# Kernel tuning notes

Hardware: AMD Instinct MI355X
Metric: run time of the kernel (lower is better)

The kernel has to match this reference:

```python
import jax, jax.numpy as jnp
import numpy as np

EPS = 1e-5

def mean_normalization(feat):
    # per (batch, channel) statistics over spatial dims, unbiased variance (torch default)
    mean = jnp.mean(feat, axis=(2, 3), keepdims=True)
    var = jnp.var(feat, axis=(2, 3), keepdims=True, ddof=1)
    return (feat - mean) / jnp.sqrt(var + EPS)

def setup_inputs() -> dict:
    key = jax.random.key(0)
    ks = jax.random.split(key, 8)
    B, C, H, W = 4, 512, 64, 64
    fan = np.sqrt(6.0 / (C + C))  # xavier_uniform gain=1 for 1x1 conv
    return {
        "content_feat": jax.random.normal(ks[0], (B, C, H, W), jnp.float32),
        "style_feat": jax.random.normal(ks[1], (B, C, H, W), jnp.float32),
        "Wq": jax.random.uniform(ks[2], (C, C), jnp.float32, -fan, fan),
        "bq": jax.random.uniform(ks[3], (C,), jnp.float32, 0.0, 1.0),
        "Wk": jax.random.uniform(ks[4], (C, C), jnp.float32, -fan, fan),
        "bk": jax.random.uniform(ks[5], (C,), jnp.float32, 0.0, 1.0),
        "Wv": jax.random.uniform(ks[6], (C, C), jnp.float32, -fan, fan),
        "bv": jax.random.uniform(ks[7], (C,), jnp.float32, 0.0, 1.0),
    }

def reference(content_feat, style_feat, Wq, bq, Wk, bk, Wv, bv):
    B, C, H, W = content_feat.shape
    N = H * W
    # 1x1 convs == channel-mixing GEMMs
    Q = jnp.einsum('oc,bchw->bohw', Wq, mean_normalization(content_feat)) + bq[None, :, None, None]
    K = jnp.einsum('oc,bchw->bohw', Wk, mean_normalization(style_feat)) + bk[None, :, None, None]
    V = jnp.einsum('oc,bchw->bohw', Wv, style_feat) + bv[None, :, None, None]
    Q = Q.reshape(B, C, N)              # [B, C, Nq]
    K = K.reshape(B, C, N)              # [B, C, Nk]
    V = V.reshape(B, C, N)              # [B, C, Nk]
    # scores[b, n, m] = Q^T K  (no 1/sqrt(d) scaling, per original)
    scores = jnp.einsum('bcn,bcm->bnm', Q, K)
    A = jax.nn.softmax(scores, axis=-1)             # [B, Nq, Nk]
    Out = jnp.einsum('bcm,bnm->bcn', V, A)          # V @ A^T
    return Out.reshape(B, C, H, W)
```

## Files before the change

kernel.cpp:

```cpp
#include <hip/hip_runtime.h>

typedef _Float16 f16;
typedef _Float16 f16x4 __attribute__((ext_vector_type(4)));
typedef _Float16 f16x8 __attribute__((ext_vector_type(8)));
typedef float f32x4 __attribute__((ext_vector_type(4)));

#define MFMA16(a, b, c) __builtin_amdgcn_mfma_f32_16x16x32_f16(a, b, c, 0, 0, 0)

__global__ __launch_bounds__(256) void stats_kernel(
    const float* __restrict__ content, const float* __restrict__ style,
    float* __restrict__ mu, float* __restrict__ rs)
{
    int bid = blockIdx.x;
    int tensor = bid >> 11;
    int row = bid & 2047;
    const float* src = (tensor ? style : content) + (size_t)row * 4096;
    int t = threadIdx.x;
    float s = 0.f, ss = 0.f;
    for (int i = t; i < 1024; i += 256) {
        float4 v = reinterpret_cast<const float4*>(src)[i];
        s  += v.x + v.y + v.z + v.w;
        ss += v.x * v.x + v.y * v.y + v.z * v.z + v.w * v.w;
    }
    for (int off = 32; off > 0; off >>= 1) {
        s  += __shfl_down(s, off);
        ss += __shfl_down(ss, off);
    }
    __shared__ float sb[4], ssb[4];
    int wv = t >> 6;
    if ((t & 63) == 0) { sb[wv] = s; ssb[wv] = ss; }
    __syncthreads();
    if (t == 0) {
        float S  = sb[0] + sb[1] + sb[2] + sb[3];
        float SS = ssb[0] + ssb[1] + ssb[2] + ssb[3];
        float m  = S * (1.f / 4096.f);
        float var = (SS - 4096.f * m * m) * (1.f / 4095.f);
        mu[bid] = m;
        rs[bid] = rsqrtf(var + 1e-5f);
    }
}

__global__ __launch_bounds__(256) void qkv_kernel(
    const float* __restrict__ content, const float* __restrict__ style,
    const float* __restrict__ Wq, const float* __restrict__ bq,
    const float* __restrict__ Wk, const float* __restrict__ bk,
    const float* __restrict__ Wv, const float* __restrict__ bv,
    const float* __restrict__ mu, const float* __restrict__ rs,
    f16* __restrict__ Qt, f16* __restrict__ Kt, f16* __restrict__ Vc)
{
    int z = blockIdx.z;
    int b = z / 3, p = z % 3;
    int n0 = blockIdx.x * 128;
    int o0 = blockIdx.y * 128;
    const float* X    = (p == 0 ? content : style) + (size_t)b * 512 * 4096;
    const float* W    = (p == 0 ? Wq : (p == 1 ? Wk : Wv));
    const float* bias = (p == 0 ? bq : (p == 1 ? bk : bv));
    const float* muT = mu + (p == 0 ? 0 : 2048) + b * 512;
    const float* rsT = rs + (p == 0 ? 0 : 2048) + b * 512;
    bool norm = (p < 2);

    __shared__ __align__(16) f16 Xt[128][40];
    __shared__ __align__(16) f16 Wl[128][40];

    int t = threadIdx.x;
    int lane = t & 63, w = t >> 6;
    int wn = (w & 1) * 64, wo = (w >> 1) * 64;
    int lg = lane >> 4, li = lane & 15;

    f32x4 acc[4][4];
#pragma unroll
    for (int i = 0; i < 4; ++i)
#pragma unroll
        for (int j = 0; j < 4; ++j)
#pragma unroll
            for (int e = 0; e < 4; ++e) acc[i][j][e] = 0.f;

    for (int kk = 0; kk < 16; ++kk) {
        int c0 = kk * 32;
        __syncthreads();
#pragma unroll
        for (int r = 0; r < 4; ++r) {
            int linear = r * 256 + t;
            int c  = linear >> 5;
            int nq = linear & 31;
            float4 v = reinterpret_cast<const float4*>(X + (size_t)(c0 + c) * 4096 + n0)[nq];
            float m = 0.f, sc = 1.f;
            if (norm) { m = muT[c0 + c]; sc = rsT[c0 + c]; }
            int n = nq * 4;
            Xt[n + 0][c] = (f16)((v.x - m) * sc);
            Xt[n + 1][c] = (f16)((v.y - m) * sc);
            Xt[n + 2][c] = (f16)((v.z - m) * sc);
            Xt[n + 3][c] = (f16)((v.w - m) * sc);
        }
#pragma unroll
        for (int r = 0; r < 4; ++r) {
            int linear = r * 256 + t;
            int o  = linear >> 3;
            int cq = linear & 7;
            float4 v = reinterpret_cast<const float4*>(W + (size_t)(o0 + o) * 512 + c0)[cq];
            int c = cq * 4;
            Wl[o][c + 0] = (f16)v.x;
            Wl[o][c + 1] = (f16)v.y;
            Wl[o][c + 2] = (f16)v.z;
            Wl[o][c + 3] = (f16)v.w;
        }
        __syncthreads();

        f16x8 xf[4], wf[4];
#pragma unroll
        for (int f = 0; f < 4; ++f) {
            xf[f] = *reinterpret_cast<const f16x8*>(&Xt[wn + f * 16 + li][lg * 8]);
            wf[f] = *reinterpret_cast<const f16x8*>(&Wl[wo + f * 16 + li][lg * 8]);
        }
        if (p < 2) {
#pragma unroll
            for (int i = 0; i < 4; ++i)
#pragma unroll
                for (int j = 0; j < 4; ++j)
                    acc[i][j] = MFMA16(wf[i], xf[j], acc[i][j]);
        } else {
#pragma unroll
            for (int i = 0; i < 4; ++i)
#pragma unroll
                for (int j = 0; j < 4; ++j)
                    acc[i][j] = MFMA16(xf[i], wf[j], acc[i][j]);
        }
    }

    if (p < 2) {
        f16* dst = (p == 0 ? Qt : Kt) + (size_t)b * 4096 * 512;
#pragma unroll
        for (int i = 0; i < 4; ++i) {
            int ob = o0 + wo + i * 16 + lg * 4;
            float4 bb = *reinterpret_cast<const float4*>(bias + ob);
#pragma unroll
            for (int j = 0; j < 4; ++j) {
                int n = n0 + wn + j * 16 + li;
                f16x4 pk;
                pk[0] = (f16)(acc[i][j][0] + bb.x);
                pk[1] = (f16)(acc[i][j][1] + bb.y);
                pk[2] = (f16)(acc[i][j][2] + bb.z);
                pk[3] = (f16)(acc[i][j][3] + bb.w);
                *reinterpret_cast<f16x4*>(dst + (size_t)n * 512 + ob) = pk;
            }
        }
    } else {
#pragma unroll
        for (int j = 0; j < 4; ++j) {
            int o = o0 + wo + j * 16 + li;
            float bb = bias[o];
            f16* dst = Vc + ((size_t)b * 512 + o) * 4096;
#pragma unroll
            for (int i = 0; i < 4; ++i) {
                int n = n0 + wn + i * 16 + lg * 4;
                f16x4 pk;
#pragma unroll
                for (int e = 0; e < 4; ++e) pk[e] = (f16)(acc[i][j][e] + bb);
                *reinterpret_cast<f16x4*>(dst + n) = pk;
            }
        }
    }
}

__global__ __launch_bounds__(768, 3) void attn_kernel(
    const f16* __restrict__ Qt, const f16* __restrict__ Kt,
    const f16* __restrict__ Vc, float* __restrict__ out)
{
    int bid = blockIdx.x;
    int orig = (bid & 7) * 32 + (bid >> 3);
    int b = orig >> 6;
    int n0 = (orig & 63) * 64;

    int t = threadIdx.x;
    int lane = t & 63, w = t >> 6;
    int lg = lane >> 4, li = lane & 15;

    __shared__ __align__(16) f16 Km[2][64][528];
    __shared__ __align__(16) f16 Pl[2][64][68];
    __shared__ __align__(16) float Rrow[2][64];
    __shared__ __align__(16) float Lrow[64];
    __shared__ int Rflag[2][4];

    const f16* Qb = Qt + (size_t)b * 4096 * 512;
    const f16* Kb = Kt + (size_t)b * 4096 * 512;
    const f16* Vb = Vc + (size_t)b * 512 * 4096;

    if (w < 4) {
        int j = w;
        f16x8 qf[16];
#pragma unroll
        for (int kk = 0; kk < 16; ++kk)
            qf[kk] = *reinterpret_cast<const f16x8*>(
                Qb + (size_t)(n0 + j * 16 + li) * 512 + kk * 32 + lg * 8);

#define STAGEK(TILE)                                                           \
        {                                                                      \
            int _db = (TILE) & 1;                                              \
            _Pragma("unroll")                                                  \
            for (int r = 0; r < 16; ++r) {                                     \
                const f16* _gs = Kb + ((size_t)(TILE) * 64 + j * 16 + r) * 512 \
                                 + lane * 8;                                   \
                __builtin_amdgcn_global_load_lds(                              \
                    (const __attribute__((address_space(1))) void*)_gs,        \
                    (__attribute__((address_space(3))) void*)&Km[_db][j * 16 + r][0], \
                    16, 0, 0);                                                 \
            }                                                                  \
        }

        STAGEK(0);
        float Mreg = -3.4e38f, Lreg = 0.f;
        __syncthreads();

        for (int it = 0; it <= 64; ++it) {
            if (it <= 63) {
                int cur = it & 1;
                if (it < 63) STAGEK(it + 1);

                f32x4 s[4];
#pragma unroll
                for (int mg = 0; mg < 4; ++mg)
#pragma unroll
                    for (int e = 0; e < 4; ++e) s[mg][e] = 0.f;
                __builtin_amdgcn_s_setprio(1);
#pragma unroll
                for (int kk = 0; kk < 16; ++kk) {
#pragma unroll
                    for (int mg = 0; mg < 4; ++mg) {
                        f16x8 kf = *reinterpret_cast<const f16x8*>(
                            &Km[cur][mg * 16 + li][kk * 32 + lg * 8]);
                        s[mg] = MFMA16(kf, qf[kk], s[mg]);
                    }
                }
                __builtin_amdgcn_s_setprio(0);

                float mx = s[0][0];
#pragma unroll
                for (int mg = 0; mg < 4; ++mg)
#pragma unroll
                    for (int e = 0; e < 4; ++e) mx = fmaxf(mx, s[mg][e]);
                mx = fmaxf(mx, __shfl_xor(mx, 16));
                mx = fmaxf(mx, __shfl_xor(mx, 32));
                bool needR = (mx - Mreg) > 4.0f;
                float Mnew = needR ? mx : Mreg;
                float r = needR ? __expf(Mreg - Mnew) : 1.f;
                float p[4][4];
                float sum = 0.f;
#pragma unroll
                for (int mg = 0; mg < 4; ++mg)
#pragma unroll
                    for (int e = 0; e < 4; ++e) {
                        p[mg][e] = __expf(s[mg][e] - Mnew);
                        sum += p[mg][e];
                    }
                sum += __shfl_xor(sum, 16);
                sum += __shfl_xor(sum, 32);
                Lreg = Lreg * r + sum;
                Mreg = Mnew;

#pragma unroll
                for (int mg = 0; mg < 4; ++mg) {
                    f16x4 pk;
#pragma unroll
                    for (int e = 0; e < 4; ++e) pk[e] = (f16)p[mg][e];
                    *reinterpret_cast<f16x4*>(&Pl[cur][j * 16 + li][mg * 16 + lg * 4]) = pk;
                }
                if (lg == 0) Rrow[cur][j * 16 + li] = r;
                int any = __any(needR);
                if (lane == 0) Rflag[cur][j] = any;
                if (it == 63 && lg == 0) Lrow[j * 16 + li] = Lreg;
            }
            __syncthreads();
        }
#undef STAGEK
    } else {
        int pw = w - 4;
        int c0 = pw * 64;
        f32x4 acc[4][4];
#pragma unroll
        for (int fn = 0; fn < 4; ++fn)
#pragma unroll
            for (int fc = 0; fc < 4; ++fc)
#pragma unroll
                for (int e = 0; e < 4; ++e) acc[fn][fc][e] = 0.f;
        f16x8 vfr[4][2];

        __syncthreads();

        for (int it = 0; it <= 64; ++it) {
            if (it >= 1) {
                int pp = (it - 1) & 1;
                if (Rflag[pp][0] | Rflag[pp][1] | Rflag[pp][2] | Rflag[pp][3]) {
#pragma unroll
                    for (int fn = 0; fn < 4; ++fn) {
                        f32x4 rv = *reinterpret_cast<const f32x4*>(&Rrow[pp][fn * 16 + lg * 4]);
#pragma unroll
                        for (int fc = 0; fc < 4; ++fc)
#pragma unroll
                            for (int e = 0; e < 4; ++e) acc[fn][fc][e] *= rv[e];
                    }
                }
                __builtin_amdgcn_s_setprio(1);
#pragma unroll
                for (int fn = 0; fn < 4; ++fn) {
                    f16x8 af0 = *reinterpret_cast<const f16x8*>(&Pl[pp][fn * 16 + li][lg * 8]);
                    f16x8 af1 = *reinterpret_cast<const f16x8*>(&Pl[pp][fn * 16 + li][32 + lg * 8]);
#pragma unroll
                    for (int fc = 0; fc < 4; ++fc) {
                        acc[fn][fc] = MFMA16(af0, vfr[fc][0], acc[fn][fc]);
                        acc[fn][fc] = MFMA16(af1, vfr[fc][1], acc[fn][fc]);
                    }
                }
                __builtin_amdgcn_s_setprio(0);
            }
            if (it <= 63) {
                const f16* vs = Vb + (size_t)(c0 + li) * 4096 + it * 64 + lg * 8;
#pragma unroll
                for (int fc = 0; fc < 4; ++fc) {
                    vfr[fc][0] = *reinterpret_cast<const f16x8*>(vs + (size_t)fc * 16 * 4096);
                    vfr[fc][1] = *reinterpret_cast<const f16x8*>(vs + (size_t)fc * 16 * 4096 + 32);
                }
            }
            __syncthreads();
        }

        float* ob = out + (size_t)b * 512 * 4096;
#pragma unroll
        for (int fn = 0; fn < 4; ++fn) {
            f32x4 lv = *reinterpret_cast<const f32x4*>(&Lrow[fn * 16 + lg * 4]);
            f32x4 linv;
#pragma unroll
            for (int e = 0; e < 4; ++e) linv[e] = 1.f / lv[e];
#pragma unroll
            for (int fc = 0; fc < 4; ++fc) {
                int c = c0 + fc * 16 + li;
                f32x4 o4;
#pragma unroll
                for (int e = 0; e < 4; ++e) o4[e] = acc[fn][fc][e] * linv[e];
                *reinterpret_cast<f32x4*>(ob + (size_t)c * 4096 + n0 + fn * 16 + lg * 4) = o4;
            }
        }
    }
}

extern "C" void kernel_launch(void* const* d_in, const int* in_sizes, int n_in,
                              void* d_out, int out_size, void* d_ws, size_t ws_size,
                              hipStream_t stream)
{
    const float* content = (const float*)d_in[0];
    const float* style   = (const float*)d_in[1];
    const float* Wq = (const float*)d_in[2];
    const float* bq = (const float*)d_in[3];
    const float* Wk = (const float*)d_in[4];
    const float* bk = (const float*)d_in[5];
    const float* Wv = (const float*)d_in[6];
    const float* bv = (const float*)d_in[7];
    float* out = (float*)d_out;

    const size_t TEN = (size_t)4 * 4096 * 512;
    f16* Qt = (f16*)d_ws;
    f16* Kt = Qt + TEN;
    f16* Vc = Kt + TEN;
    float* mu = (float*)(Vc + TEN);
    float* rs = mu + 4096;

    hipLaunchKernelGGL(stats_kernel, dim3(4096), dim3(256), 0, stream,
                       content, style, mu, rs);
    hipLaunchKernelGGL(qkv_kernel, dim3(32, 4, 12), dim3(256), 0, stream,
                       content, style, Wq, bq, Wk, bk, Wv, bv, mu, rs, Qt, Kt, Vc);
    hipLaunchKernelGGL(attn_kernel, dim3(256), dim3(768), 0, stream,
                       Qt, Kt, Vc, out);
}
```

Measured before the change: 302.0 us.

## Pre-convert weights to fp16 and restructure QKV GEMM to stage full-K activation tile

Adds a kernel that converts Wq/Wk/Wv to fp16 once per call. The QKV projection now has each block handle 64 spatial positions across all 512 output channels. The block loads the whole normalized 64x512 activation tile into shared memory once, and each wave streams fp16 weight fragments straight from global memory. This removes the per-K-step shared-memory staging, the repeated fp32 weight conversion and the per-iteration barriers. The costs are an extra launch, weight reads served from global/L2 instead of shared memory, and a larger shared allocation that may limit occupancy.

```diff
diff --git a/kernel.cpp b/kernel.cpp
--- a/kernel.cpp
+++ b/kernel.cpp
@@ -40,33 +40,69 @@
     }
 }
 
-__global__ __launch_bounds__(256) void qkv_kernel(
+__global__ __launch_bounds__(256) void wcvt_kernel(
+    const float* __restrict__ Wq, const float* __restrict__ Wk,
+    const float* __restrict__ Wv, f16* __restrict__ Wh)
+{
+    int p = blockIdx.y;
+    const float* W = (p == 0 ? Wq : (p == 1 ? Wk : Wv));
+    f16* dst = Wh + (size_t)p * 262144;
+    int base = blockIdx.x * 256 + threadIdx.x;
+#pragma unroll
+    for (int i = 0; i < 8; ++i) {
+        int e4 = i * 8192 + base;
+        float4 v = reinterpret_cast<const float4*>(W)[e4];
+        f16x4 pk;
+        pk[0] = (f16)v.x; pk[1] = (f16)v.y; pk[2] = (f16)v.z; pk[3] = (f16)v.w;
+        reinterpret_cast<f16x4*>(dst)[e4] = pk;
+    }
+}
+
+__global__ __launch_bounds__(512, 3) void qkv_kernel(
     const float* __restrict__ content, const float* __restrict__ style,
-    const float* __restrict__ Wq, const float* __restrict__ bq,
-    const float* __restrict__ Wk, const float* __restrict__ bk,
-    const float* __restrict__ Wv, const float* __restrict__ bv,
+    const f16* __restrict__ Wh,
+    const float* __restrict__ bq, const float* __restrict__ bk,
+    const float* __restrict__ bv,
     const float* __restrict__ mu, const float* __restrict__ rs,
     f16* __restrict__ Qt, f16* __restrict__ Kt, f16* __restrict__ Vc)
 {
-    int z = blockIdx.z;
-    int b = z / 3, p = z % 3;
-    int n0 = blockIdx.x * 128;
-    int o0 = blockIdx.y * 128;
+    int nb = blockIdx.x;
+    int y  = blockIdx.y;
+    int b = y / 3, p = y % 3;
+    int n0 = nb * 64;
     const float* X    = (p == 0 ? content : style) + (size_t)b * 512 * 4096;
-    const float* W    = (p == 0 ? Wq : (p == 1 ? Wk : Wv));
+    const f16*   Wp   = Wh + (size_t)p * 262144;
     const float* bias = (p == 0 ? bq : (p == 1 ? bk : bv));
-    const float* muT = mu + (p == 0 ? 0 : 2048) + b * 512;
-    const float* rsT = rs + (p == 0 ? 0 : 2048) + b * 512;
+    const float* muT  = mu + (p == 0 ? 0 : 2048) + b * 512;
+    const float* rsT  = rs + (p == 0 ? 0 : 2048) + b * 512;
     bool norm = (p < 2);
 
-    __shared__ __align__(16) f16 Xt[128][40];
-    __shared__ __align__(16) f16 Wl[128][40];
+    __shared__ __align__(16) f16 Xt[64][520];
 
     int t = threadIdx.x;
     int lane = t & 63, w = t >> 6;
-    int wn = (w & 1) * 64, wo = (w >> 1) * 64;
     int lg = lane >> 4, li = lane & 15;
 
+#pragma unroll
+    for (int i = 0; i < 16; ++i) {
+        int c0 = i * 32 + w * 4;
+        float x0 = X[(size_t)(c0 + 0) * 4096 + n0 + lane];
+        float x1 = X[(size_t)(c0 + 1) * 4096 + n0 + lane];
+        float x2 = X[(size_t)(c0 + 2) * 4096 + n0 + lane];
+        float x3 = X[(size_t)(c0 + 3) * 4096 + n0 + lane];
+        f16x4 pk;
+        if (norm) {
+            pk[0] = (f16)((x0 - muT[c0 + 0]) * rsT[c0 + 0]);
+            pk[1] = (f16)((x1 - muT[c0 + 1]) * rsT[c0 + 1]);
+            pk[2] = (f16)((x2 - muT[c0 + 2]) * rsT[c0 + 2]);
+            pk[3] = (f16)((x3 - muT[c0 + 3]) * rsT[c0 + 3]);
+        } else {
+            pk[0] = (f16)x0; pk[1] = (f16)x1; pk[2] = (f16)x2; pk[3] = (f16)x3;
+        }
+        *reinterpret_cast<f16x4*>(&Xt[lane][c0]) = pk;
+    }
+    __syncthreads();
+
     f32x4 acc[4][4];
 #pragma unroll
     for (int i = 0; i < 4; ++i)
@@ -75,87 +111,59 @@
 #pragma unroll
             for (int e = 0; e < 4; ++e) acc[i][j][e] = 0.f;
 
+    const f16* wbase = Wp + (size_t)(w * 64 + li) * 512 + lg * 8;
     for (int kk = 0; kk < 16; ++kk) {
-        int c0 = kk * 32;
-        __syncthreads();
-#pragma unroll
-        for (int r = 0; r < 4; ++r) {
-            int linear = r * 256 + t;
-            int c  = linear >> 5;
-            int nq = linear & 31;
-            float4 v = reinterpret_cast<const float4*>(X + (size_t)(c0 + c) * 4096 + n0)[nq];
-            float m = 0.f, sc = 1.f;
-            if (norm) { m = muT[c0 + c]; sc = rsT[c0 + c]; }
-            int n = nq * 4;
-            Xt[n + 0][c] = (f16)((v.x - m) * sc);
-            Xt[n + 1][c] = (f16)((v.y - m) * sc);
-            Xt[n + 2][c] = (f16)((v.z - m) * sc);
-            Xt[n + 3][c] = (f16)((v.w - m) * sc);
-        }
-#pragma unroll
-        for (int r = 0; r < 4; ++r) {
-            int linear = r * 256 + t;
-            int o  = linear >> 3;
-            int cq = linear & 7;
-            float4 v = reinterpret_cast<const float4*>(W + (size_t)(o0 + o) * 512 + c0)[cq];
-            int c = cq * 4;
-            Wl[o][c + 0] = (f16)v.x;
-            Wl[o][c + 1] = (f16)v.y;
-            Wl[o][c + 2] = (f16)v.z;
-            Wl[o][c + 3] = (f16)v.w;
-        }
-        __syncthreads();
-
         f16x8 xf[4], wf[4];
 #pragma unroll
-        for (int f = 0; f < 4; ++f) {
-            xf[f] = *reinterpret_cast<const f16x8*>(&Xt[wn + f * 16 + li][lg * 8]);
-            wf[f] = *reinterpret_cast<const f16x8*>(&Wl[wo + f * 16 + li][lg * 8]);
-        }
+        for (int jn = 0; jn < 4; ++jn)
+            xf[jn] = *reinterpret_cast<const f16x8*>(&Xt[jn * 16 + li][kk * 32 + lg * 8]);
+#pragma unroll
+        for (int io = 0; io < 4; ++io)
+            wf[io] = *reinterpret_cast<const f16x8*>(wbase + (size_t)io * 16 * 512 + kk * 32);
         if (p < 2) {
 #pragma unroll
-            for (int i = 0; i < 4; ++i)
-#pragma unroll
-                for (int j = 0; j < 4; ++j)
-                    acc[i][j] = MFMA16(wf[i], xf[j], acc[i][j]);
+            for (int io = 0; io < 4; ++io)
+#pragma unroll
+                for (int jn = 0; jn < 4; ++jn)
+                    acc[io][jn] = MFMA16(wf[io], xf[jn], acc[io][jn]);
         } else {
 #pragma unroll
-            for (int i = 0; i < 4; ++i)
-#pragma unroll
-                for (int j = 0; j < 4; ++j)
-                    acc[i][j] = MFMA16(xf[i], wf[j], acc[i][j]);
+            for (int jn = 0; jn < 4; ++jn)
+#pragma unroll
+                for (int io = 0; io < 4; ++io)
+                    acc[jn][io] = MFMA16(xf[jn], wf[io], acc[jn][io]);
         }
     }
 
     if (p < 2) {
         f16* dst = (p == 0 ? Qt : Kt) + (size_t)b * 4096 * 512;
 #pragma unroll
-        for (int i = 0; i < 4; ++i) {
-            int ob = o0 + wo + i * 16 + lg * 4;
+        for (int io = 0; io < 4; ++io) {
+            int ob = w * 64 + io * 16 + lg * 4;
             float4 bb = *reinterpret_cast<const float4*>(bias + ob);
 #pragma unroll
-            for (int j = 0; j < 4; ++j) {
-                int n = n0 + wn + j * 16 + li;
+            for (int jn = 0; jn < 4; ++jn) {
+                int n = n0 + jn * 16 + li;
                 f16x4 pk;
-                pk[0] = (f16)(acc[i][j][0] + bb.x);
-                pk[1] = (f16)(acc[i][j][1] + bb.y);
-                pk[2] = (f16)(acc[i][j][2] + bb.z);
-                pk[3] = (f16)(acc[i][j][3] + bb.w);
+                pk[0] = (f16)(acc[io][jn][0] + bb.x);
+                pk[1] = (f16)(acc[io][jn][1] + bb.y);
+                pk[2] = (f16)(acc[io][jn][2] + bb.z);
+                pk[3] = (f16)(acc[io][jn][3] + bb.w);
                 *reinterpret_cast<f16x4*>(dst + (size_t)n * 512 + ob) = pk;
             }
         }
     } else {
 #pragma unroll
-        for (int j = 0; j < 4; ++j) {
-            int o = o0 + wo + j * 16 + li;
+        for (int io = 0; io < 4; ++io) {
+            int o = w * 64 + io * 16 + li;
             float bb = bias[o];
             f16* dst = Vc + ((size_t)b * 512 + o) * 4096;
 #pragma unroll
-            for (int i = 0; i < 4; ++i) {
-                int n = n0 + wn + i * 16 + lg * 4;
+            for (int jn = 0; jn < 4; ++jn) {
+                int n = n0 + jn * 16 + lg * 4;
                 f16x4 pk;
 #pragma unroll
-                for (int e = 0; e < 4; ++e) pk[e] = (f16)(acc[i][j][e] + bb);
+                for (int e = 0; e < 4; ++e) pk[e] = (f16)(acc[jn][io][e] + bb);
                 *reinterpret_cast<f16x4*>(dst + n) = pk;
             }
         }
@@ -362,11 +370,14 @@
     f16* Vc = Kt + TEN;
     float* mu = (float*)(Vc + TEN);
     float* rs = mu + 4096;
+    f16* Wh = (f16*)(rs + 4096);
 
     hipLaunchKernelGGL(stats_kernel, dim3(4096), dim3(256), 0, stream,
                        content, style, mu, rs);
-    hipLaunchKernelGGL(qkv_kernel, dim3(32, 4, 12), dim3(256), 0, stream,
-                       content, style, Wq, bq, Wk, bk, Wv, bv, mu, rs, Qt, Kt, Vc);
+    hipLaunchKernelGGL(wcvt_kernel, dim3(32, 3), dim3(256), 0, stream,
+                       Wq, Wk, Wv, Wh);
+    hipLaunchKernelGGL(qkv_kernel, dim3(64, 12), dim3(512), 0, stream,
+                       content, style, Wh, bq, bk, bv, mu, rs, Qt, Kt, Vc);
     hipLaunchKernelGGL(attn_kernel, dim3(256), dim3(768), 0, stream,
                        Qt, Kt, Vc, out);
 }
```

After: 250.6 us (median of 2 runs). 17.0% less time.
